# Performance work log

Measured on AMD Instinct MI355X. Metric: run time of the kernel, lower is better.

## Reference

```python
import jax, jax.numpy as jnp
import numpy as np

D = 512      # word_embedding_dim (dim_in == dim_out)
HEADS = 8    # isab_num_heads
M = 16       # isab_num_inds
B = 2048     # batch_news_num = batch_size * news_num
S = 32       # max_title_length
EPS = 1e-5   # torch LayerNorm default eps


def _layer_norm(x, g, b):
    mu = jnp.mean(x, axis=-1, keepdims=True)
    var = jnp.mean((x - mu) ** 2, axis=-1, keepdims=True)
    return (x - mu) * jax.lax.rsqrt(var + EPS) * g + b


def _mab(Qin, Kin, Wqkv, bqkv, Wo, bo, g0, b0, g1, b1):
    # Faithful to torch MAB: linear Q/K/V, head split via reshape (equivalent
    # to split/cat since cat-back restores head slices), scale by sqrt(dim_V).
    d = Wqkv.shape[-1]
    Q = Qin @ Wqkv[0] + bqkv[0]          # [B, Sq, d]
    K = Kin @ Wqkv[1] + bqkv[1]          # [B, Sk, d]
    V = Kin @ Wqkv[2] + bqkv[2]
    Bn, Sq, _ = Q.shape
    Sk = K.shape[1]
    hd = d // HEADS
    Qh = Q.reshape(Bn, Sq, HEADS, hd)
    Kh = K.reshape(Bn, Sk, HEADS, hd)
    Vh = V.reshape(Bn, Sk, HEADS, hd)
    scores = jnp.einsum('bqhd,bkhd->bhqk', Qh, Kh) / jnp.sqrt(jnp.asarray(d, Q.dtype))
    A = jax.nn.softmax(scores, axis=-1)
    Oh = Qh + jnp.einsum('bhqk,bkhd->bqhd', A, Vh)   # residual on Q_
    O = Oh.reshape(Bn, Sq, d)
    O = _layer_norm(O, g0, b0)                        # ln0
    O = O + jax.nn.relu(O @ Wo + bo)                  # O + relu(fc_o(O))
    O = _layer_norm(O, g1, b1)                        # ln1
    return O


def _isab(X, I, p0, p1):
    Iq = jnp.broadcast_to(I, (X.shape[0],) + I.shape[1:])  # I.repeat(B,1,1)
    Hm = _mab(Iq, X, *p0)   # mab0(I, X) -> [B, M, d]
    return _mab(X, Hm, *p1)  # mab1(X, H) -> [B, S, d]


def setup_inputs() -> dict:
    key = jax.random.key(0)
    ks = jax.random.split(key, 12)
    sc = 1.0 / np.sqrt(D)
    inp = {
        'x': jax.random.normal(ks[0], (B, S, D), dtype=jnp.float32),
        'I': jax.random.normal(ks[1], (1, M, D), dtype=jnp.float32) * sc,
        'mab0_Wqkv': jax.random.normal(ks[2], (3, D, D), dtype=jnp.float32) * sc,
        'mab0_bqkv': jnp.zeros((3, D), dtype=jnp.float32),
        'mab0_Wo': jax.random.normal(ks[3], (D, D), dtype=jnp.float32) * sc,
        'mab0_bo': jnp.zeros((D,), dtype=jnp.float32),
        'mab0_g0': jnp.ones((D,), dtype=jnp.float32),
        'mab0_b0': jnp.zeros((D,), dtype=jnp.float32),
        'mab0_g1': jnp.ones((D,), dtype=jnp.float32),
        'mab0_b1': jnp.zeros((D,), dtype=jnp.float32),
        'mab1_Wqkv': jax.random.normal(ks[4], (3, D, D), dtype=jnp.float32) * sc,
        'mab1_bqkv': jnp.zeros((3, D), dtype=jnp.float32),
        'mab1_Wo': jax.random.normal(ks[5], (D, D), dtype=jnp.float32) * sc,
        'mab1_bo': jnp.zeros((D,), dtype=jnp.float32),
        'mab1_g0': jnp.ones((D,), dtype=jnp.float32),
        'mab1_b0': jnp.zeros((D,), dtype=jnp.float32),
        'mab1_g1': jnp.ones((D,), dtype=jnp.float32),
        'mab1_b1': jnp.zeros((D,), dtype=jnp.float32),
    }
    return inp


def reference(x, I,
              mab0_Wqkv, mab0_bqkv, mab0_Wo, mab0_bo, mab0_g0, mab0_b0, mab0_g1, mab0_b1,
              mab1_Wqkv, mab1_bqkv, mab1_Wo, mab1_bo, mab1_g0, mab1_b0, mab1_g1, mab1_b1):
    p0 = (mab0_Wqkv, mab0_bqkv, mab0_Wo, mab0_bo, mab0_g0, mab0_b0, mab0_g1, mab0_b1)
    p1 = (mab1_Wqkv, mab1_bqkv, mab1_Wo, mab1_bo, mab1_g0, mab1_b0, mab1_g1, mab1_b1)
    # CIDER title path (eval mode, dropout=identity): ISAB applied twice, mean pool
    h1 = _isab(x, I, p0, p1)
    h2 = _isab(h1, I, p0, p1)
    return jnp.mean(h2, axis=1)   # [B, D] title_embedding
```

## Files before the change

kernel.cpp:

```cpp
#include <hip/hip_runtime.h>
#include <hip/hip_bf16.h>

#define D 512
#define BATCH 2048
#define SEQ 32
#define MIND 16

typedef __hip_bfloat16 bf16;
typedef __attribute__((ext_vector_type(8))) short s8v;
typedef __attribute__((ext_vector_type(4))) short s4v;
typedef __attribute__((ext_vector_type(4))) float f4v;

#define SWZ(row, kb) (((row) << 10) + ((kb) ^ (((row) & 7) << 4)))

__device__ __forceinline__ ushort f2bu(float f) {
    bf16 h = __float2bfloat16(f); ushort u; __builtin_memcpy(&u, &h, 2); return u;
}
__device__ __forceinline__ float bu2f(ushort u) {
    unsigned x = ((unsigned)u) << 16; float f; __builtin_memcpy(&f, &x, 4); return f;
}

__device__ __forceinline__ float wave_sum(float v) {
#pragma unroll
    for (int off = 32; off >= 1; off >>= 1) v += __shfl_xor(v, off, 64);
    return v;
}


template <int BM, bool SPARSEA, bool AF32>
__device__ __forceinline__ void stage_A(char* sA, const ushort* __restrict__ Ab,
                                        const float* __restrict__ Af, size_t m0, int tid) {
    for (int c = tid; c < BM * 64; c += 512) {
        const int row = c >> 6, k8 = (c & 63) << 3;
        const size_t L = m0 + row;
        const size_t pr = SPARSEA ? ((L >> 4) * 32 + (L & 15)) : L;
        s8v o;
        if constexpr (AF32) {
            const float* src = Af + pr * D + k8;
            const f4v v0 = __builtin_nontemporal_load((const f4v*)src);
            const f4v v1 = __builtin_nontemporal_load((const f4v*)(src + 4));
            o = s8v{(short)f2bu(v0.x), (short)f2bu(v0.y), (short)f2bu(v0.z), (short)f2bu(v0.w),
                    (short)f2bu(v1.x), (short)f2bu(v1.y), (short)f2bu(v1.z), (short)f2bu(v1.w)};
        } else {
            o = *(const s8v*)(Ab + pr * D + k8);
        }
        *(s8v*)(sA + SWZ(row, k8 * 2)) = o;
    }
}

template <int BM>
__device__ __forceinline__ void ln_sA(char* sA, const float* __restrict__ lng,
                                      const float* __restrict__ lnb, int lane, int wv) {
    for (int i = wv; i < BM; i += 8) {
        float v[8];
#pragma unroll
        for (int j = 0; j < 8; ++j)
            v[j] = bu2f(*(const ushort*)(sA + SWZ(i, 2 * (lane + 64 * j))));
        float s = 0.f;
#pragma unroll
        for (int j = 0; j < 8; ++j) s += v[j];
        s = wave_sum(s);
        const float mu = s * (1.f / 512.f);
        float q2 = 0.f;
#pragma unroll
        for (int j = 0; j < 8; ++j) { const float t = v[j] - mu; q2 = fmaf(t, t, q2); }
        q2 = wave_sum(q2);
        const float inv = rsqrtf(q2 * (1.f / 512.f) + 1e-5f);
#pragma unroll
        for (int j = 0; j < 8; ++j) {
            const int d0 = lane + 64 * j;
            *(ushort*)(sA + SWZ(i, 2 * d0)) = f2bu((v[j] - mu) * inv * lng[d0] + lnb[d0]);
        }
    }
}

template <int RT>
__device__ __forceinline__ void run_kloop(const char* sA, const ushort* __restrict__ Wt,
                                          int m, int g, int swm, int wv, f4v (*acc)[4]) {
    const ushort* Bp = Wt + ((size_t)(wv * 64 + m) << 9) + 8 * g;
    s8v b0[4], b1[4], b2[4];
#pragma unroll
    for (int ct = 0; ct < 4; ++ct) b0[ct] = *(const s8v*)(Bp + ct * 8192);
#pragma unroll
    for (int ct = 0; ct < 4; ++ct) b1[ct] = *(const s8v*)(Bp + ct * 8192 + 32);
#pragma unroll
    for (int k0 = 0; k0 < 512; k0 += 32) {
        if (k0 < 448) {
#pragma unroll
            for (int ct = 0; ct < 4; ++ct) b2[ct] = *(const s8v*)(Bp + ct * 8192 + k0 + 64);
        }
        const int kb = 2 * (k0 + 8 * g);
        s8v a[RT];
#pragma unroll
        for (int rt = 0; rt < RT; ++rt)
            a[rt] = *(const s8v*)(sA + ((rt * 16 + m) << 10) + (kb ^ swm));
#pragma unroll
        for (int ct = 0; ct < 4; ++ct)
#pragma unroll
            for (int rt = 0; rt < RT; ++rt)
                acc[rt][ct] = __builtin_amdgcn_mfma_f32_16x16x32_bf16(a[rt], b0[ct], acc[rt][ct], 0, 0, 0);
#pragma unroll
        for (int ct = 0; ct < 4; ++ct) { b0[ct] = b1[ct]; b1[ct] = b2[ct]; }
    }
}

struct WPtrs { const float* s[7]; };

__global__ __launch_bounds__(256) void wtrans7(WPtrs wp, ushort* __restrict__ Wt) {
    const float* W = wp.s[blockIdx.z];
    ushort* dst = Wt + (size_t)blockIdx.z * 262144;
    __shared__ float t[32][33];
    const int k0 = blockIdx.x * 32, n0 = blockIdx.y * 32;
    const int lx = threadIdx.x & 31, ly = threadIdx.x >> 5;
    for (int i = ly; i < 32; i += 8) t[i][lx] = W[(size_t)(k0 + i) * D + n0 + lx];
    __syncthreads();
    for (int i = ly; i < 32; i += 8)
        dst[(size_t)(n0 + i) * D + k0 + lx] = f2bu(t[lx][i]);
}

__global__ __launch_bounds__(256) void q0_kernel(
    const float* __restrict__ I, const float* __restrict__ Wq,
    const float* __restrict__ bq, ushort* __restrict__ Q0b)
{
    const int q = blockIdx.x;
    const int c = threadIdx.x;
    float a0 = 0.f, a1 = 0.f;
    for (int k = 0; k < D; ++k) {
        const float iv = I[q * D + k];
        a0 = fmaf(iv, Wq[(size_t)k * D + c], a0);
        a1 = fmaf(iv, Wq[(size_t)k * D + c + 256], a1);
    }
    Q0b[q * D + c]       = f2bu(a0 + bq[c]);
    Q0b[q * D + c + 256] = f2bu(a1 + bq[c + 256]);
}

template <int BM, int NOUT, bool RESFUSE, bool LNA, bool SPARSEA, bool AF32>
__global__ __launch_bounds__(512, 4) void gemmN(
    const ushort* __restrict__ Ab, const float* __restrict__ Af,
    const ushort* __restrict__ Wt0, const float* __restrict__ bias0, ushort* __restrict__ C0,
    const ushort* __restrict__ Wt1, const float* __restrict__ bias1, ushort* __restrict__ C1,
    const ushort* __restrict__ Wt2, const float* __restrict__ bias2, ushort* __restrict__ C2,
    const float* __restrict__ lng, const float* __restrict__ lnb)
{
    constexpr int RT = BM / 16;
    __shared__ __align__(16) char sA[BM * 1024];
    __shared__ __align__(16) char sC[16 * 1024];
    const int tid = threadIdx.x, lane = tid & 63, wv = tid >> 6;
    const size_t m0 = (size_t)blockIdx.x * BM;

    stage_A<BM, SPARSEA, AF32>(sA, Ab, Af, m0, tid);
    __syncthreads();
    if constexpr (LNA) { ln_sA<BM>(sA, lng, lnb, lane, wv); __syncthreads(); }

    const int m = lane & 15, g = lane >> 4;
    const int swm = (m & 7) << 4;
    const ushort* Wts[3]  = {Wt0, Wt1, Wt2};
    const float*  bias[3] = {bias0, bias1, bias2};
    ushort*       Cs[3]   = {C0, C1, C2};

#pragma unroll
    for (int o = 0; o < NOUT; ++o) {
        f4v acc[RT][4];
#pragma unroll
        for (int i = 0; i < RT; ++i)
#pragma unroll
            for (int j = 0; j < 4; ++j) acc[i][j] = (f4v){0.f, 0.f, 0.f, 0.f};
        run_kloop<RT>(sA, Wts[o], m, g, swm, wv, acc);

        ushort* Cb = Cs[o];
        const float* bb = bias[o];
#pragma unroll
        for (int rt = 0; rt < RT; ++rt) {
            __syncthreads();
#pragma unroll
            for (int ct = 0; ct < 4; ++ct) {
                const int col = wv * 64 + ct * 16 + m;
                const float bv = bb[col];
#pragma unroll
                for (int r = 0; r < 4; ++r) {
                    const int lrow = g * 4 + r;
                    float v = acc[rt][ct][r] + bv;
                    if (RESFUSE)
                        v = bu2f(*(const ushort*)(sA + SWZ(rt * 16 + lrow, 2 * col))) + fmaxf(v, 0.f);
                    *(ushort*)(sC + SWZ(lrow, 2 * col)) = f2bu(v);
                }
            }
            __syncthreads();
            for (int c = tid; c < 16 * 64; c += 512) {
                const int row = c >> 6, k8 = (c & 63) << 3;
                *(s8v*)(Cb + (m0 + rt * 16 + row) * D + k8) = *(const s8v*)(sC + SWZ(row, k8 * 2));
            }
        }
        __syncthreads();
    }
}

template <int SQ, int SK, bool QSHARED, int OSTR>
__global__ __launch_bounds__(64) void attn_core(
    const ushort* __restrict__ Qb, const ushort* __restrict__ Kb,
    const ushort* __restrict__ Vb, ushort* __restrict__ Ob)
{
    constexpr int RS = 72;
    __shared__ __align__(16) ushort sQ[SQ * RS];
    __shared__ __align__(16) ushort sK[SK * RS];
    __shared__ __align__(16) ushort sV[SK * RS];
    __shared__ float sS[SQ][SK + 1];

    const int lane = threadIdx.x;
    const int b = blockIdx.x, h = blockIdx.y;
    const size_t qbase = (QSHARED ? (size_t)0 : (size_t)b * SQ * D) + h * 64;
    const size_t kbase = (size_t)b * SK * D + h * 64;

    for (int idx = lane; idx < SQ * 16; idx += 64) {
        const int r = idx >> 4, c4 = (idx & 15) << 2;
        *(s4v*)(sQ + r * RS + c4) = *(const s4v*)(Qb + qbase + (size_t)r * D + c4);
    }
    for (int idx = lane; idx < SK * 16; idx += 64) {
        const int r = idx >> 4, c4 = (idx & 15) << 2;
        *(s4v*)(sK + r * RS + c4) = *(const s4v*)(Kb + kbase + (size_t)r * D + c4);
        *(s4v*)(sV + r * RS + c4) = *(const s4v*)(Vb + kbase + (size_t)r * D + c4);
    }
    __syncthreads();

    const float scale = 0.044194173824159216f;
#pragma unroll
    for (int o = 0; o < SQ * SK / 64; ++o) {
        const int idx = o * 64 + lane;
        const int q = idx / SK, k = idx % SK;
        float s = 0.f;
#pragma unroll
        for (int dd = 0; dd < 64; dd += 8) {
            const s8v aq = *(const s8v*)(sQ + q * RS + dd);
            const s8v ak = *(const s8v*)(sK + k * RS + dd);
#pragma unroll
            for (int e = 0; e < 8; ++e)
                s = fmaf(bu2f((ushort)aq[e]), bu2f((ushort)ak[e]), s);
        }
        sS[q][k] = s * scale;
    }
    __syncthreads();

    if (lane < SQ) {
        float* row = sS[lane];
        float mx = row[0];
#pragma unroll
        for (int k = 1; k < SK; ++k) mx = fmaxf(mx, row[k]);
        float sum = 0.f;
#pragma unroll
        for (int k = 0; k < SK; ++k) { const float e = __expf(row[k] - mx); row[k] = e; sum += e; }
        const float inv = 1.f / sum;
#pragma unroll
        for (int k = 0; k < SK; ++k) row[k] *= inv;
    }
    __syncthreads();

    float acc[SQ];
#pragma unroll
    for (int q = 0; q < SQ; ++q) acc[q] = 0.f;
#pragma unroll 4
    for (int k = 0; k < SK; ++k) {
        const float v = bu2f(sV[k * RS + lane]);
#pragma unroll
        for (int q = 0; q < SQ; ++q) acc[q] = fmaf(sS[q][k], v, acc[q]);
    }
    const size_t obase = (size_t)b * OSTR * D + h * 64 + lane;
#pragma unroll
    for (int q = 0; q < SQ; ++q)
        Ob[obase + (size_t)q * D] = f2bu(bu2f(sQ[q * RS + lane]) + acc[q]);
}

__global__ __launch_bounds__(512) void ln_meanpool(
    const ushort* __restrict__ U, const float* __restrict__ gg,
    const float* __restrict__ bb, float* __restrict__ outp)
{
    __shared__ float sP[8][512];
    const int tid = threadIdx.x, lane = tid & 63, wv = tid >> 6;
    const size_t b = blockIdx.x;
    float a[8];
#pragma unroll
    for (int j = 0; j < 8; ++j) a[j] = 0.f;
    for (int i = wv; i < 32; i += 8) {
        const ushort* u = U + ((size_t)b * 32 + i) * D;
        float v[8];
#pragma unroll
        for (int j = 0; j < 8; ++j) v[j] = bu2f(u[lane + 64 * j]);
        float s = 0.f;
#pragma unroll
        for (int j = 0; j < 8; ++j) s += v[j];
        s = wave_sum(s);
        const float mu = s * (1.f / 512.f);
        float q2 = 0.f;
#pragma unroll
        for (int j = 0; j < 8; ++j) { const float t = v[j] - mu; q2 = fmaf(t, t, q2); }
        q2 = wave_sum(q2);
        const float inv = rsqrtf(q2 * (1.f / 512.f) + 1e-5f);
#pragma unroll
        for (int j = 0; j < 8; ++j) {
            const int d0 = lane + 64 * j;
            a[j] += (v[j] - mu) * inv * gg[d0] + bb[d0];
        }
    }
#pragma unroll
    for (int j = 0; j < 8; ++j) sP[wv][lane + 64 * j] = a[j];
    __syncthreads();
    float s = 0.f;
#pragma unroll
    for (int w = 0; w < 8; ++w) s += sP[w][tid];
    outp[b * D + tid] = s * (1.f / 32.f);
}

extern "C" void kernel_launch(void* const* d_in, const int* in_sizes, int n_in,
                              void* d_out, int out_size, void* d_ws, size_t ws_size,
                              hipStream_t stream) {
    (void)in_sizes; (void)n_in; (void)out_size; (void)ws_size;

    const float* x     = (const float*)d_in[0];
    const float* I     = (const float*)d_in[1];
    const float* W0    = (const float*)d_in[2];
    const float* bqkv0 = (const float*)d_in[3];
    const float* Wo0   = (const float*)d_in[4];
    const float* bo0   = (const float*)d_in[5];
    const float* g00   = (const float*)d_in[6];
    const float* b00   = (const float*)d_in[7];
    const float* g01   = (const float*)d_in[8];
    const float* b01   = (const float*)d_in[9];
    const float* W1    = (const float*)d_in[10];
    const float* bqkv1 = (const float*)d_in[11];
    const float* Wo1   = (const float*)d_in[12];
    const float* bo1   = (const float*)d_in[13];
    const float* g10   = (const float*)d_in[14];
    const float* b10   = (const float*)d_in[15];
    const float* g11   = (const float*)d_in[16];
    const float* b11   = (const float*)d_in[17];

    const float* Wq0 = W0;     const float* Wk0 = W0 + D * D;  const float* Wv0 = W0 + 2 * D * D;
    const float* bq0 = bqkv0;  const float* bk0 = bqkv0 + D;   const float* bv0 = bqkv0 + 2 * D;
    const float* Wq1 = W1;     const float* Wk1 = W1 + D * D;  const float* Wv1 = W1 + 2 * D * D;
    const float* bq1 = bqkv1;  const float* bk1 = bqkv1 + D;   const float* bv1 = bqkv1 + 2 * D;

    char* ws = (char*)d_ws;
    ushort* Q0b = (ushort*)ws;
    ushort* Wt  = (ushort*)(ws + 32768);
    char* base = ws + 32768 + 7 * 524288;
    ushort* P0 = (ushort*)(base);
    ushort* P1 = (ushort*)(base + ((size_t)64 << 20));
    ushort* P2 = (ushort*)(base + ((size_t)128 << 20));
    ushort* P3 = (ushort*)(base + ((size_t)192 << 20));
    const size_t HALFE = (size_t)16 << 20;
    ushort* P1hi = P1 + HALFE;

    ushort* WtK0 = Wt + 0 * 262144;
    ushort* WtV0 = Wt + 1 * 262144;
    ushort* WtO0 = Wt + 2 * 262144;
    ushort* WtQ1 = Wt + 3 * 262144;
    ushort* WtK1 = Wt + 4 * 262144;
    ushort* WtV1 = Wt + 5 * 262144;
    ushort* WtO1 = Wt + 6 * 262144;

    WPtrs wp; wp.s[0] = Wk0; wp.s[1] = Wv0; wp.s[2] = Wo0; wp.s[3] = Wq1;
    wp.s[4] = Wk1; wp.s[5] = Wv1; wp.s[6] = Wo1;
    wtrans7<<<dim3(16, 16, 7), 256, 0, stream>>>(wp, Wt);
    q0_kernel<<<MIND, 256, 0, stream>>>(I, Wq0, bq0, Q0b);

    constexpr int GBS = BATCH * SEQ / 64;
    constexpr int GBM = BATCH * MIND / 64;
    const dim3 ag(BATCH, 8);

    for (int isab = 0; isab < 2; ++isab) {
        if (isab == 0)
            gemmN<64, 3, false, false, false, true><<<GBS, 512, 0, stream>>>(
                nullptr, x, WtK0, bk0, P1, WtV0, bv0, P2, WtQ1, bq1, P3, nullptr, nullptr);
        else
            gemmN<64, 3, false, true, false, false><<<GBS, 512, 0, stream>>>(
                P0, nullptr, WtK0, bk0, P1, WtV0, bv0, P2, WtQ1, bq1, P3, g11, b11);
        attn_core<MIND, SEQ, true, 32><<<ag, 64, 0, stream>>>(Q0b, P1, P2, P1);
        gemmN<64, 1, true, true, true, false><<<GBM, 512, 0, stream>>>(
            P1, nullptr, WtO0, bo0, P2, nullptr, nullptr, nullptr, nullptr, nullptr, nullptr, g00, b00);
        gemmN<64, 2, false, true, false, false><<<GBM, 512, 0, stream>>>(
            P2, nullptr, WtK1, bk1, P1, WtV1, bv1, P1hi, nullptr, nullptr, nullptr, g01, b01);
        attn_core<SEQ, MIND, false, 32><<<ag, 64, 0, stream>>>(P3, P1, P1hi, P3);
        gemmN<64, 1, true, true, false, false><<<GBS, 512, 0, stream>>>(
            P3, nullptr, WtO1, bo1, P0, nullptr, nullptr, nullptr, nullptr, nullptr, nullptr, g10, b10);
    }

    ln_meanpool<<<BATCH, 512, 0, stream>>>(P0, g11, b11, (float*)d_out);
}
```

Before: 1.485 ms.

## Use 128-row tiles for QKV GEMM, simplify B prefetch, nontemporal loads/stores

The fused 3-output projection GEMM now processes 128 rows per block with a lower occupancy target, which doubles reuse of each weight fragment loaded from global memory. The register-rotating B-operand prefetch pipeline is replaced by a plain per-step load, freeing registers at the cost of exposed load latency. Activation loads and output stores become nontemporal to reduce cache pollution. The larger tile doubles LDS use and accumulator registers, lowering occupancy.

```diff
diff --git a/kernel.cpp b/kernel.cpp
--- a/kernel.cpp
+++ b/kernel.cpp
@@ -42,7 +42,7 @@
             o = s8v{(short)f2bu(v0.x), (short)f2bu(v0.y), (short)f2bu(v0.z), (short)f2bu(v0.w),
                     (short)f2bu(v1.x), (short)f2bu(v1.y), (short)f2bu(v1.z), (short)f2bu(v1.w)};
         } else {
-            o = *(const s8v*)(Ab + pr * D + k8);
+            o = __builtin_nontemporal_load((const s8v*)(Ab + pr * D + k8));
         }
         *(s8v*)(sA + SWZ(row, k8 * 2)) = o;
     }
@@ -78,17 +78,11 @@
 __device__ __forceinline__ void run_kloop(const char* sA, const ushort* __restrict__ Wt,
                                           int m, int g, int swm, int wv, f4v (*acc)[4]) {
     const ushort* Bp = Wt + ((size_t)(wv * 64 + m) << 9) + 8 * g;
-    s8v b0[4], b1[4], b2[4];
-#pragma unroll
-    for (int ct = 0; ct < 4; ++ct) b0[ct] = *(const s8v*)(Bp + ct * 8192);
-#pragma unroll
-    for (int ct = 0; ct < 4; ++ct) b1[ct] = *(const s8v*)(Bp + ct * 8192 + 32);
 #pragma unroll
     for (int k0 = 0; k0 < 512; k0 += 32) {
-        if (k0 < 448) {
-#pragma unroll
-            for (int ct = 0; ct < 4; ++ct) b2[ct] = *(const s8v*)(Bp + ct * 8192 + k0 + 64);
-        }
+        s8v bfr[4];
+#pragma unroll
+        for (int ct = 0; ct < 4; ++ct) bfr[ct] = *(const s8v*)(Bp + ct * 8192 + k0);
         const int kb = 2 * (k0 + 8 * g);
         s8v a[RT];
 #pragma unroll
@@ -98,10 +92,39 @@
         for (int ct = 0; ct < 4; ++ct)
 #pragma unroll
             for (int rt = 0; rt < RT; ++rt)
-                acc[rt][ct] = __builtin_amdgcn_mfma_f32_16x16x32_bf16(a[rt], b0[ct], acc[rt][ct], 0, 0, 0);
-#pragma unroll
-        for (int ct = 0; ct < 4; ++ct) { b0[ct] = b1[ct]; b1[ct] = b2[ct]; }
-    }
+                acc[rt][ct] = __builtin_amdgcn_mfma_f32_16x16x32_bf16(a[rt], bfr[ct], acc[rt][ct], 0, 0, 0);
+    }
+}
+
+template <int RT, bool RESFUSE>
+__device__ __forceinline__ void epilogue_out(const f4v (*acc)[4], const float* __restrict__ bb,
+                                             const char* sA, char* sC, ushort* __restrict__ Cb,
+                                             size_t m0, int tid, int lane, int wv) {
+    const int m = lane & 15, g = lane >> 4;
+#pragma unroll
+    for (int rt = 0; rt < RT; ++rt) {
+        __syncthreads();
+#pragma unroll
+        for (int ct = 0; ct < 4; ++ct) {
+            const int col = wv * 64 + ct * 16 + m;
+            const float bv = bb[col];
+#pragma unroll
+            for (int r = 0; r < 4; ++r) {
+                const int lrow = g * 4 + r;
+                float v = acc[rt][ct][r] + bv;
+                if (RESFUSE)
+                    v = bu2f(*(const ushort*)(sA + SWZ(rt * 16 + lrow, 2 * col))) + fmaxf(v, 0.f);
+                *(ushort*)(sC + SWZ(lrow, 2 * col)) = f2bu(v);
+            }
+        }
+        __syncthreads();
+        for (int c = tid; c < 16 * 64; c += 512) {
+            const int row = c >> 6, k8 = (c & 63) << 3;
+            __builtin_nontemporal_store(*(const s8v*)(sC + SWZ(row, k8 * 2)),
+                                        (s8v*)(Cb + (m0 + rt * 16 + row) * D + k8));
+        }
+    }
+    __syncthreads();
 }
 
 struct WPtrs { const float* s[7]; };
@@ -134,8 +157,8 @@
     Q0b[q * D + c + 256] = f2bu(a1 + bq[c + 256]);
 }
 
-template <int BM, int NOUT, bool RESFUSE, bool LNA, bool SPARSEA, bool AF32>
-__global__ __launch_bounds__(512, 4) void gemmN(
+template <int BM, int MINW, int NOUT, bool RESFUSE, bool LNA, bool SPARSEA, bool AF32>
+__global__ __launch_bounds__(512, MINW) void gemmT(
     const ushort* __restrict__ Ab, const float* __restrict__ Af,
     const ushort* __restrict__ Wt0, const float* __restrict__ bias0, ushort* __restrict__ C0,
     const ushort* __restrict__ Wt1, const float* __restrict__ bias1, ushort* __restrict__ C1,
@@ -166,32 +189,7 @@
 #pragma unroll
             for (int j = 0; j < 4; ++j) acc[i][j] = (f4v){0.f, 0.f, 0.f, 0.f};
         run_kloop<RT>(sA, Wts[o], m, g, swm, wv, acc);
-
-        ushort* Cb = Cs[o];
-        const float* bb = bias[o];
-#pragma unroll
-        for (int rt = 0; rt < RT; ++rt) {
-            __syncthreads();
-#pragma unroll
-            for (int ct = 0; ct < 4; ++ct) {
-                const int col = wv * 64 + ct * 16 + m;
-                const float bv = bb[col];
-#pragma unroll
-                for (int r = 0; r < 4; ++r) {
-                    const int lrow = g * 4 + r;
-                    float v = acc[rt][ct][r] + bv;
-                    if (RESFUSE)
-                        v = bu2f(*(const ushort*)(sA + SWZ(rt * 16 + lrow, 2 * col))) + fmaxf(v, 0.f);
-                    *(ushort*)(sC + SWZ(lrow, 2 * col)) = f2bu(v);
-                }
-            }
-            __syncthreads();
-            for (int c = tid; c < 16 * 64; c += 512) {
-                const int row = c >> 6, k8 = (c & 63) << 3;
-                *(s8v*)(Cb + (m0 + rt * 16 + row) * D + k8) = *(const s8v*)(sC + SWZ(row, k8 * 2));
-            }
-        }
-        __syncthreads();
+        epilogue_out<RT, RESFUSE>(acc, bias[o], sA, sC, Cs[o], m0, tid, lane, wv);
     }
 }
 
@@ -362,24 +360,25 @@
     wtrans7<<<dim3(16, 16, 7), 256, 0, stream>>>(wp, Wt);
     q0_kernel<<<MIND, 256, 0, stream>>>(I, Wq0, bq0, Q0b);
 
+    constexpr int GW  = BATCH * SEQ / 128;
     constexpr int GBS = BATCH * SEQ / 64;
     constexpr int GBM = BATCH * MIND / 64;
     const dim3 ag(BATCH, 8);
 
     for (int isab = 0; isab < 2; ++isab) {
         if (isab == 0)
-            gemmN<64, 3, false, false, false, true><<<GBS, 512, 0, stream>>>(
+            gemmT<128, 2, 3, false, false, false, true><<<GW, 512, 0, stream>>>(
                 nullptr, x, WtK0, bk0, P1, WtV0, bv0, P2, WtQ1, bq1, P3, nullptr, nullptr);
         else
-            gemmN<64, 3, false, true, false, false><<<GBS, 512, 0, stream>>>(
+            gemmT<128, 2, 3, false, true, false, false><<<GW, 512, 0, stream>>>(
                 P0, nullptr, WtK0, bk0, P1, WtV0, bv0, P2, WtQ1, bq1, P3, g11, b11);
         attn_core<MIND, SEQ, true, 32><<<ag, 64, 0, stream>>>(Q0b, P1, P2, P1);
-        gemmN<64, 1, true, true, true, false><<<GBM, 512, 0, stream>>>(
+        gemmT<64, 4, 1, true, true, true, false><<<GBM, 512, 0, stream>>>(
             P1, nullptr, WtO0, bo0, P2, nullptr, nullptr, nullptr, nullptr, nullptr, nullptr, g00, b00);
-        gemmN<64, 2, false, true, false, false><<<GBM, 512, 0, stream>>>(
+        gemmT<64, 4, 2, false, true, false, false><<<GBM, 512, 0, stream>>>(
             P2, nullptr, WtK1, bk1, P1, WtV1, bv1, P1hi, nullptr, nullptr, nullptr, g01, b01);
         attn_core<SEQ, MIND, false, 32><<<ag, 64, 0, stream>>>(P3, P1, P1hi, P3);
-        gemmN<64, 1, true, true, false, false><<<GBS, 512, 0, stream>>>(
+        gemmT<64, 4, 1, true, true, false, false><<<GBS, 512, 0, stream>>>(
             P3, nullptr, WtO1, bo1, P0, nullptr, nullptr, nullptr, nullptr, nullptr, nullptr, g10, b10);
     }
 
```

Result: faster. 1.340 ms (-9.8%).
